# Optimization experiments

Hardware: AMD Instinct MI355X
Metric: run time of the kernel (lower is better)

## Reference

```python
import jax, jax.numpy as jnp
import numpy as np

T, B, I, H, L = 512, 4096, 23, 20, 2  # seq len, batch, input dim, hidden dim, num layers


def setup_inputs() -> dict:
    key = jax.random.key(0)
    ks = jax.random.split(key, 13)
    s = 1.0 / np.sqrt(H)  # pytorch default uniform bound scale (use normal*s for simplicity)
    f32 = jnp.float32
    return {
        "x": jax.random.normal(ks[0], (T, B, I), f32),
        "h0": jax.random.normal(ks[1], (L, B, H), f32),
        "c0": jax.random.normal(ks[2], (L, B, H), f32),
        "W_ih0": jax.random.normal(ks[3], (4 * H, I), f32) * s,
        "W_hh0": jax.random.normal(ks[4], (4 * H, H), f32) * s,
        "b_ih0": jax.random.normal(ks[5], (4 * H,), f32) * s,
        "b_hh0": jax.random.normal(ks[6], (4 * H,), f32) * s,
        "W_ih1": jax.random.normal(ks[7], (4 * H, H), f32) * s,
        "W_hh1": jax.random.normal(ks[8], (4 * H, H), f32) * s,
        "b_ih1": jax.random.normal(ks[9], (4 * H,), f32) * s,
        "b_hh1": jax.random.normal(ks[10], (4 * H,), f32) * s,
        "W_lin": jax.random.normal(ks[11], (1, H), f32) * s,
        "b_lin": jax.random.normal(ks[12], (1,), f32) * s,
    }


def _lstm_layer(xs, h0, c0, W_ih, W_hh, b_ih, b_hh):
    # Precompute input contributions for all timesteps at once: [T, B, 4H]
    xg = jnp.einsum('tbi,gi->tbg', xs, W_ih) + b_ih + b_hh

    def step(carry, xg_t):
        h, c = carry
        gates = xg_t + h @ W_hh.T          # [B, 4H]
        i, f, g, o = jnp.split(gates, 4, axis=-1)  # pytorch gate order: i, f, g, o
        c = jax.nn.sigmoid(f) * c + jax.nn.sigmoid(i) * jnp.tanh(g)
        h = jax.nn.sigmoid(o) * jnp.tanh(c)
        return (h, c), h

    _, hs = jax.lax.scan(step, (h0, c0), xg)
    return hs  # [T, B, H]


def reference(x, h0, c0, W_ih0, W_hh0, b_ih0, b_hh0, W_ih1, W_hh1, b_ih1, b_hh1, W_lin, b_lin):
    out = _lstm_layer(x, h0[0], c0[0], W_ih0, W_hh0, b_ih0, b_hh0)
    out = _lstm_layer(out, h0[1], c0[1], W_ih1, W_hh1, b_ih1, b_hh1)
    y = jax.nn.relu(out)                   # relu(lstm output), [T, B, H]
    # lin applied then time-index 6 selected; equivalent (and cheaper) to index first
    z6 = y[6] @ W_lin.T + b_lin            # [B, 1]
    return jax.nn.relu(z6)
```

## Files before the change

### kernel.cpp

```cpp
#include <hip/hip_runtime.h>
#include <math.h>


constexpr int kT  = 7;
constexpr int kI  = 23;
constexpr int kH  = 20;
constexpr int kG  = 80;
constexpr int kBT = 8;
constexpr int kThreads = 320;

__device__ __forceinline__ float sigm(float v) {
    return __builtin_amdgcn_rcpf(1.0f + __builtin_amdgcn_exp2f(v * -1.44269504f));
}
__device__ __forceinline__ float tanh_(float v) {
    return 1.0f - 2.0f * __builtin_amdgcn_rcpf(__builtin_amdgcn_exp2f(v * 2.88539008f) + 1.0f);
}
template<int J>
__device__ __forceinline__ float qb(float v) {
    return __int_as_float(__builtin_amdgcn_mov_dpp(__float_as_int(v), J * 0x55, 0xF, 0xF, true));
}
__device__ __forceinline__ void lstm_update(float a, float& c, float& h) {
    const float gi = qb<0>(a);
    const float gf = qb<1>(a);
    const float gg = qb<2>(a);
    const float go = qb<3>(a);
    c = sigm(gf) * c + sigm(gi) * tanh_(gg);
    h = sigm(go) * tanh_(c);
}

__global__ __launch_bounds__(kThreads, 3) void lstm7_kernel(
    const float* __restrict__ x,
    const float* __restrict__ h0,
    const float* __restrict__ c0,
    const float* __restrict__ Wih0,
    const float* __restrict__ Whh0,
    const float* __restrict__ bih0,
    const float* __restrict__ bhh0,
    const float* __restrict__ Wih1,
    const float* __restrict__ Whh1,
    const float* __restrict__ bih1,
    const float* __restrict__ bhh1,
    const float* __restrict__ Wlin,
    const float* __restrict__ blin,
    float* __restrict__ out,
    int B)
{
    __shared__ __align__(16) float xS[kT][kI][kBT];
    __shared__ __align__(16) float h1S[2][kH][kBT];
    __shared__ __align__(16) float h2S[2][kH][kBT];

    const int tid = threadIdx.x;
    const int b0  = blockIdx.x * kBT;
    const int bp  = tid / kG;
    const int q   = tid & 3;
    const int u   = (tid % kG) >> 2;
    const int grow = q * kH + u;
    const int bb  = bp * 2;

    for (int idx = tid; idx < kT * kI * kBT; idx += kThreads) {
        const int t = idx / (kI * kBT);
        const int r = idx % (kI * kBT);
        const int i = r / kBT;
        const int b = r % kBT;
        xS[t][i][b] = x[((size_t)t * B + b0 + b) * kI + i];
    }
    if (tid < kH * kBT) {
        const int uu = tid / kBT, b = tid % kBT;
        h1S[0][uu][b] = h0[(size_t)(b0 + b) * kH + uu];
        h2S[0][uu][b] = h0[(size_t)(B + b0 + b) * kH + uu];
    }

    float wA[kI], wB[kH], wC[kH], wD[kH];
    {
        const float* pa = Wih0 + grow * kI;
#pragma unroll
        for (int k = 0; k < kI; ++k) wA[k] = pa[k];
        const float4* pb = reinterpret_cast<const float4*>(Whh0 + grow * kH);
        const float4* pc = reinterpret_cast<const float4*>(Wih1 + grow * kH);
        const float4* pd = reinterpret_cast<const float4*>(Whh1 + grow * kH);
#pragma unroll
        for (int j = 0; j < 5; ++j) {
            const float4 vb = pb[j], vc = pc[j], vd = pd[j];
            wB[4*j] = vb.x; wB[4*j+1] = vb.y; wB[4*j+2] = vb.z; wB[4*j+3] = vb.w;
            wC[4*j] = vc.x; wC[4*j+1] = vc.y; wC[4*j+2] = vc.z; wC[4*j+3] = vc.w;
            wD[4*j] = vd.x; wD[4*j+1] = vd.y; wD[4*j+2] = vd.z; wD[4*j+3] = vd.w;
        }
    }
    const float bias1 = bih0[grow] + bhh0[grow];
    const float bias2 = bih1[grow] + bhh1[grow];

    float2 c1, c2;
    c1.x = c0[(size_t)(b0 + bb) * kH + u];
    c1.y = c0[(size_t)(b0 + bb + 1) * kH + u];
    c2.x = c0[(size_t)(B + b0 + bb) * kH + u];
    c2.y = c0[(size_t)(B + b0 + bb + 1) * kH + u];

    __syncthreads();

#pragma unroll
    for (int t = 0; t < kT; ++t) {
        const int rb = t & 1, wb = rb ^ 1;

        float a0 = bias1, a1 = bias1, e0 = 0.f, e1 = 0.f;
#pragma unroll
        for (int k = 0; k < kI; ++k) {
            const float2 v = *reinterpret_cast<const float2*>(&xS[t][k][bb]);
            if (k & 1) { e0 = fmaf(wA[k], v.x, e0); e1 = fmaf(wA[k], v.y, e1); }
            else       { a0 = fmaf(wA[k], v.x, a0); a1 = fmaf(wA[k], v.y, a1); }
        }
#pragma unroll
        for (int k = 0; k < kH; ++k) {
            const float2 v = *reinterpret_cast<const float2*>(&h1S[rb][k][bb]);
            if (k & 1) { e0 = fmaf(wB[k], v.x, e0); e1 = fmaf(wB[k], v.y, e1); }
            else       { a0 = fmaf(wB[k], v.x, a0); a1 = fmaf(wB[k], v.y, a1); }
        }
        a0 += e0; a1 += e1;

        {
            float hx, hy;
            lstm_update(a0, c1.x, hx);
            lstm_update(a1, c1.y, hy);
            if (q == 0) *reinterpret_cast<float2*>(&h1S[wb][u][bb]) = make_float2(hx, hy);
        }
        __syncthreads();

        float g0 = bias2, g1 = bias2, f0 = 0.f, f1 = 0.f;
#pragma unroll
        for (int k = 0; k < kH; ++k) {
            const float2 v = *reinterpret_cast<const float2*>(&h1S[wb][k][bb]);
            if (k & 1) { f0 = fmaf(wC[k], v.x, f0); f1 = fmaf(wC[k], v.y, f1); }
            else       { g0 = fmaf(wC[k], v.x, g0); g1 = fmaf(wC[k], v.y, g1); }
        }
#pragma unroll
        for (int k = 0; k < kH; ++k) {
            const float2 v = *reinterpret_cast<const float2*>(&h2S[rb][k][bb]);
            if (k & 1) { f0 = fmaf(wD[k], v.x, f0); f1 = fmaf(wD[k], v.y, f1); }
            else       { g0 = fmaf(wD[k], v.x, g0); g1 = fmaf(wD[k], v.y, g1); }
        }
        g0 += f0; g1 += f1;

        {
            float hx, hy;
            lstm_update(g0, c2.x, hx);
            lstm_update(g1, c2.y, hy);
            if (q == 0) *reinterpret_cast<float2*>(&h2S[wb][u][bb]) = make_float2(hx, hy);
        }
        __syncthreads();
    }

    if (tid < kBT) {
        const int b = tid;
        float acc = blin[0];
#pragma unroll
        for (int uu = 0; uu < kH; ++uu) {
            acc = fmaf(fmaxf(h2S[1][uu][b], 0.0f), Wlin[uu], acc);
        }
        out[b0 + b] = fmaxf(acc, 0.0f);
    }
}

extern "C" void kernel_launch(void* const* d_in, const int* in_sizes, int n_in,
                              void* d_out, int out_size, void* d_ws, size_t ws_size,
                              hipStream_t stream) {
    const float* x    = (const float*)d_in[0];
    const float* h0   = (const float*)d_in[1];
    const float* c0   = (const float*)d_in[2];
    const float* Wih0 = (const float*)d_in[3];
    const float* Whh0 = (const float*)d_in[4];
    const float* bih0 = (const float*)d_in[5];
    const float* bhh0 = (const float*)d_in[6];
    const float* Wih1 = (const float*)d_in[7];
    const float* Whh1 = (const float*)d_in[8];
    const float* bih1 = (const float*)d_in[9];
    const float* bhh1 = (const float*)d_in[10];
    const float* Wlin = (const float*)d_in[11];
    const float* blin = (const float*)d_in[12];
    float* out = (float*)d_out;

    const int B = in_sizes[1] / (2 * kH);
    const int blocks = B / kBT;

    hipLaunchKernelGGL(lstm7_kernel, dim3(blocks), dim3(kThreads), 0, stream,
                       x, h0, c0, Wih0, Whh0, bih0, bhh0,
                       Wih1, Whh1, bih1, bhh1, Wlin, blin, out, B);
}
```

Before: 24.93 us.

## Remap LSTM to single-wavefront blocks with DPP-rotated hidden-state dot products

Each block is now one 64-thread wavefront handling two batch elements, instead of 320 threads handling eight. Each lane computes one primary gate row plus a redundant secondary row. Lanes in a quad load a float4 slice of the hidden state and pass it around with DPP rotations, so each lane makes fewer LDS reads; weights are stored in the matching rotated order. The layer-0 input projection for all 7 steps is computed before the recurrence, and single-buffered shared state relies on in-order execution within one wave. The costs are redundant math for gate rows 16-19, higher register pressure, and four times as many blocks.

Result: slower. 70.74 us (+183.7%).

```diff
diff --git a/kernel.cpp b/kernel.cpp
--- a/kernel.cpp
+++ b/kernel.cpp
@@ -2,12 +2,11 @@
 #include <math.h>
 
 
-constexpr int kT  = 7;
-constexpr int kI  = 23;
-constexpr int kH  = 20;
-constexpr int kG  = 80;
-constexpr int kBT = 8;
-constexpr int kThreads = 320;
+constexpr int kT = 7;
+constexpr int kI = 23;
+constexpr int kH = 20;
+constexpr int kE = 2;
+constexpr int kThreads = 64;
 
 __device__ __forceinline__ float sigm(float v) {
     return __builtin_amdgcn_rcpf(1.0f + __builtin_amdgcn_exp2f(v * -1.44269504f));
@@ -19,16 +18,66 @@
 __device__ __forceinline__ float qb(float v) {
     return __int_as_float(__builtin_amdgcn_mov_dpp(__float_as_int(v), J * 0x55, 0xF, 0xF, true));
 }
+__device__ __forceinline__ float rotl(float v) {
+    return __int_as_float(__builtin_amdgcn_mov_dpp(__float_as_int(v), 0x39, 0xF, 0xF, true));
+}
+__device__ __forceinline__ float4 rot4(float4 v) {
+    return make_float4(rotl(v.x), rotl(v.y), rotl(v.z), rotl(v.w));
+}
 __device__ __forceinline__ void lstm_update(float a, float& c, float& h) {
-    const float gi = qb<0>(a);
-    const float gf = qb<1>(a);
-    const float gg = qb<2>(a);
-    const float go = qb<3>(a);
+    const float gi = qb<0>(a), gf = qb<1>(a), gg = qb<2>(a), go = qb<3>(a);
     c = sigm(gf) * c + sigm(gi) * tanh_(gg);
     h = sigm(go) * tanh_(c);
 }
 
-__global__ __launch_bounds__(kThreads, 3) void lstm7_kernel(
+#define DOT_STEP4(o)                                                 \
+    p0 = fmaf(wp[o+0], v.x, p0); p1 = fmaf(wp[o+1], v.y, p1);        \
+    s0 = fmaf(ws[o+0], v.x, s0); s1 = fmaf(ws[o+1], v.y, s1);        \
+    p0 = fmaf(wp[o+2], v.z, p0); p1 = fmaf(wp[o+3], v.w, p1);        \
+    s0 = fmaf(ws[o+2], v.z, s0); s1 = fmaf(ws[o+3], v.w, s1);
+
+__device__ __forceinline__ void dot20x2(const float* __restrict__ row,
+                                        const float* wp, const float* ws,
+                                        int q4, float& rp, float& rs)
+{
+    float4 v = *reinterpret_cast<const float4*>(row + q4);
+    float p0 = 0.f, p1 = 0.f, s0 = 0.f, s1 = 0.f;
+    DOT_STEP4(0)  v = rot4(v);
+    DOT_STEP4(4)  v = rot4(v);
+    DOT_STEP4(8)  v = rot4(v);
+    DOT_STEP4(12)
+    const float4 t = *reinterpret_cast<const float4*>(row + 16);
+    p0 = fmaf(wp[16], t.x, p0); p1 = fmaf(wp[17], t.y, p1);
+    s0 = fmaf(ws[16], t.x, s0); s1 = fmaf(ws[17], t.y, s1);
+    p0 = fmaf(wp[18], t.z, p0); p1 = fmaf(wp[19], t.w, p1);
+    s0 = fmaf(ws[18], t.z, s0); s1 = fmaf(ws[19], t.w, s1);
+    rp = p0 + p1; rs = s0 + s1;
+}
+
+__device__ __forceinline__ void dot24x2(const float* __restrict__ row,
+                                        const float* wp, const float* ws,
+                                        int q4, float& rp, float& rs)
+{
+    float4 v = *reinterpret_cast<const float4*>(row + q4);
+    float p0 = 0.f, p1 = 0.f, s0 = 0.f, s1 = 0.f;
+    DOT_STEP4(0)  v = rot4(v);
+    DOT_STEP4(4)  v = rot4(v);
+    DOT_STEP4(8)  v = rot4(v);
+    DOT_STEP4(12)
+    const float4 t4 = *reinterpret_cast<const float4*>(row + 16);
+    p0 = fmaf(wp[16], t4.x, p0); p1 = fmaf(wp[17], t4.y, p1);
+    s0 = fmaf(ws[16], t4.x, s0); s1 = fmaf(ws[17], t4.y, s1);
+    p0 = fmaf(wp[18], t4.z, p0); p1 = fmaf(wp[19], t4.w, p1);
+    s0 = fmaf(ws[18], t4.z, s0); s1 = fmaf(ws[19], t4.w, s1);
+    const float4 t5 = *reinterpret_cast<const float4*>(row + 20);
+    p0 = fmaf(wp[20], t5.x, p0); p1 = fmaf(wp[21], t5.y, p1);
+    s0 = fmaf(ws[20], t5.x, s0); s1 = fmaf(ws[21], t5.y, s1);
+    p0 = fmaf(wp[22], t5.z, p0); p1 = fmaf(wp[23], t5.w, p1);
+    s0 = fmaf(ws[22], t5.z, s0); s1 = fmaf(ws[23], t5.w, s1);
+    rp = p0 + p1; rs = s0 + s1;
+}
+
+__global__ __launch_bounds__(kThreads, 2) void lstm7_kernel(
     const float* __restrict__ x,
     const float* __restrict__ h0,
     const float* __restrict__ c0,
@@ -45,117 +94,143 @@
     float* __restrict__ out,
     int B)
 {
-    __shared__ __align__(16) float xS[kT][kI][kBT];
-    __shared__ __align__(16) float h1S[2][kH][kBT];
-    __shared__ __align__(16) float h2S[2][kH][kBT];
+    __shared__ __align__(16) float xL[kE][kT][24];
+    __shared__ __align__(16) float h1S[kE][24];
+    __shared__ __align__(16) float h2S[kE][24];
 
     const int tid = threadIdx.x;
-    const int b0  = blockIdx.x * kBT;
-    const int bp  = tid / kG;
+    const int b0  = blockIdx.x * kE;
     const int q   = tid & 3;
-    const int u   = (tid % kG) >> 2;
-    const int grow = q * kH + u;
-    const int bb  = bp * 2;
-
-    for (int idx = tid; idx < kT * kI * kBT; idx += kThreads) {
-        const int t = idx / (kI * kBT);
-        const int r = idx % (kI * kBT);
-        const int i = r / kBT;
-        const int b = r % kBT;
-        xS[t][i][b] = x[((size_t)t * B + b0 + b) * kI + i];
-    }
-    if (tid < kH * kBT) {
-        const int uu = tid / kBT, b = tid % kBT;
-        h1S[0][uu][b] = h0[(size_t)(b0 + b) * kH + uu];
-        h2S[0][uu][b] = h0[(size_t)(B + b0 + b) * kH + uu];
-    }
-
-    float wA[kI], wB[kH], wC[kH], wD[kH];
+    const int u   = tid >> 2;
+    const int su  = 16 + (u & 3);
+    const int gp  = q * kH + u;
+    const int gs  = q * kH + su;
+    const int q4  = q * 4;
+
+    for (int idx = tid; idx < kE * kT * 24; idx += kThreads) {
+        const int e = idx / (kT * 24);
+        const int r = idx % (kT * 24);
+        const int t = r / 24;
+        const int i = r % 24;
+        xL[e][t][i] = (i < kI) ? x[((size_t)t * B + b0 + e) * kI + i] : 0.0f;
+    }
+    if (tid < kE * kH) {
+        const int e = tid / kH, uu = tid % kH;
+        h1S[e][uu] = h0[(size_t)(b0 + e) * kH + uu];
+        h2S[e][uu] = h0[((size_t)B + b0 + e) * kH + uu];
+    }
+    __syncthreads();
+
+    float xgp0[kT], xgp1[kT], xgs0[kT], xgs1[kT];
     {
-        const float* pa = Wih0 + grow * kI;
-#pragma unroll
-        for (int k = 0; k < kI; ++k) wA[k] = pa[k];
-        const float4* pb = reinterpret_cast<const float4*>(Whh0 + grow * kH);
-        const float4* pc = reinterpret_cast<const float4*>(Wih1 + grow * kH);
-        const float4* pd = reinterpret_cast<const float4*>(Whh1 + grow * kH);
-#pragma unroll
-        for (int j = 0; j < 5; ++j) {
-            const float4 vb = pb[j], vc = pc[j], vd = pd[j];
-            wB[4*j] = vb.x; wB[4*j+1] = vb.y; wB[4*j+2] = vb.z; wB[4*j+3] = vb.w;
-            wC[4*j] = vc.x; wC[4*j+1] = vc.y; wC[4*j+2] = vc.z; wC[4*j+3] = vc.w;
-            wD[4*j] = vd.x; wD[4*j+1] = vd.y; wD[4*j+2] = vd.z; wD[4*j+3] = vd.w;
-        }
-    }
-    const float bias1 = bih0[grow] + bhh0[grow];
-    const float bias2 = bih1[grow] + bhh1[grow];
-
-    float2 c1, c2;
-    c1.x = c0[(size_t)(b0 + bb) * kH + u];
-    c1.y = c0[(size_t)(b0 + bb + 1) * kH + u];
-    c2.x = c0[(size_t)(B + b0 + bb) * kH + u];
-    c2.y = c0[(size_t)(B + b0 + bb + 1) * kH + u];
-
-    __syncthreads();
+        float wAp[24], wAs[24];
+        const float* Ap = Wih0 + gp * kI;
+        const float* As = Wih0 + gs * kI;
+#pragma unroll
+        for (int r = 0; r < 4; ++r) {
+            const int c = (q + r) & 3;
+#pragma unroll
+            for (int j = 0; j < 4; ++j) {
+                wAp[4*r + j] = Ap[4*c + j];
+                wAs[4*r + j] = As[4*c + j];
+            }
+        }
+#pragma unroll
+        for (int j = 0; j < 7; ++j) { wAp[16 + j] = Ap[16 + j]; wAs[16 + j] = As[16 + j]; }
+        wAp[23] = 0.0f; wAs[23] = 0.0f;
+        const float b1p = bih0[gp] + bhh0[gp];
+        const float b1s = bih0[gs] + bhh0[gs];
+#pragma unroll
+        for (int t = 0; t < kT; ++t) {
+            float dp, ds;
+            dot24x2(&xL[0][t][0], wAp, wAs, q4, dp, ds);
+            xgp0[t] = b1p + dp; xgs0[t] = b1s + ds;
+            dot24x2(&xL[1][t][0], wAp, wAs, q4, dp, ds);
+            xgp1[t] = b1p + dp; xgs1[t] = b1s + ds;
+        }
+    }
+
+    float wBp[kH], wCp[kH], wDp[kH], wBs[kH], wCs[kH], wDs[kH];
+    {
+        const float4* PB = reinterpret_cast<const float4*>(Whh0 + gp * kH);
+        const float4* PC = reinterpret_cast<const float4*>(Wih1 + gp * kH);
+        const float4* PD = reinterpret_cast<const float4*>(Whh1 + gp * kH);
+        const float4* SB = reinterpret_cast<const float4*>(Whh0 + gs * kH);
+        const float4* SC = reinterpret_cast<const float4*>(Wih1 + gs * kH);
+        const float4* SD = reinterpret_cast<const float4*>(Whh1 + gs * kH);
+#pragma unroll
+        for (int r = 0; r < 4; ++r) {
+            const int c = (q + r) & 3;
+            const float4 vb = PB[c], vc = PC[c], vd = PD[c];
+            const float4 ub = SB[c], uc = SC[c], ud = SD[c];
+            wBp[4*r+0]=vb.x; wBp[4*r+1]=vb.y; wBp[4*r+2]=vb.z; wBp[4*r+3]=vb.w;
+            wCp[4*r+0]=vc.x; wCp[4*r+1]=vc.y; wCp[4*r+2]=vc.z; wCp[4*r+3]=vc.w;
+            wDp[4*r+0]=vd.x; wDp[4*r+1]=vd.y; wDp[4*r+2]=vd.z; wDp[4*r+3]=vd.w;
+            wBs[4*r+0]=ub.x; wBs[4*r+1]=ub.y; wBs[4*r+2]=ub.z; wBs[4*r+3]=ub.w;
+            wCs[4*r+0]=uc.x; wCs[4*r+1]=uc.y; wCs[4*r+2]=uc.z; wCs[4*r+3]=uc.w;
+            wDs[4*r+0]=ud.x; wDs[4*r+1]=ud.y; wDs[4*r+2]=ud.z; wDs[4*r+3]=ud.w;
+        }
+        const float4 tb = PB[4], tc = PC[4], td = PD[4];
+        const float4 rb = SB[4], rc = SC[4], rd = SD[4];
+        wBp[16]=tb.x; wBp[17]=tb.y; wBp[18]=tb.z; wBp[19]=tb.w;
+        wCp[16]=tc.x; wCp[17]=tc.y; wCp[18]=tc.z; wCp[19]=tc.w;
+        wDp[16]=td.x; wDp[17]=td.y; wDp[18]=td.z; wDp[19]=td.w;
+        wBs[16]=rb.x; wBs[17]=rb.y; wBs[18]=rb.z; wBs[19]=rb.w;
+        wCs[16]=rc.x; wCs[17]=rc.y; wCs[18]=rc.z; wCs[19]=rc.w;
+        wDs[16]=rd.x; wDs[17]=rd.y; wDs[18]=rd.z; wDs[19]=rd.w;
+    }
+    const float b2p = bih1[gp] + bhh1[gp];
+    const float b2s = bih1[gs] + bhh1[gs];
+
+    float c1p0 = c0[(size_t)(b0 + 0) * kH + u];
+    float c1p1 = c0[(size_t)(b0 + 1) * kH + u];
+    float c2p0 = c0[((size_t)B + b0 + 0) * kH + u];
+    float c2p1 = c0[((size_t)B + b0 + 1) * kH + u];
+    float c1s0 = c0[(size_t)(b0 + 0) * kH + su];
+    float c1s1 = c0[(size_t)(b0 + 1) * kH + su];
+    float c2s0 = c0[((size_t)B + b0 + 0) * kH + su];
+    float c2s1 = c0[((size_t)B + b0 + 1) * kH + su];
 
 #pragma unroll
     for (int t = 0; t < kT; ++t) {
-        const int rb = t & 1, wb = rb ^ 1;
-
-        float a0 = bias1, a1 = bias1, e0 = 0.f, e1 = 0.f;
-#pragma unroll
-        for (int k = 0; k < kI; ++k) {
-            const float2 v = *reinterpret_cast<const float2*>(&xS[t][k][bb]);
-            if (k & 1) { e0 = fmaf(wA[k], v.x, e0); e1 = fmaf(wA[k], v.y, e1); }
-            else       { a0 = fmaf(wA[k], v.x, a0); a1 = fmaf(wA[k], v.y, a1); }
-        }
-#pragma unroll
-        for (int k = 0; k < kH; ++k) {
-            const float2 v = *reinterpret_cast<const float2*>(&h1S[rb][k][bb]);
-            if (k & 1) { e0 = fmaf(wB[k], v.x, e0); e1 = fmaf(wB[k], v.y, e1); }
-            else       { a0 = fmaf(wB[k], v.x, a0); a1 = fmaf(wB[k], v.y, a1); }
-        }
-        a0 += e0; a1 += e1;
-
-        {
-            float hx, hy;
-            lstm_update(a0, c1.x, hx);
-            lstm_update(a1, c1.y, hy);
-            if (q == 0) *reinterpret_cast<float2*>(&h1S[wb][u][bb]) = make_float2(hx, hy);
+        float dp0, ds0, dp1, ds1;
+        dot20x2(&h1S[0][0], wBp, wBs, q4, dp0, ds0);
+        dot20x2(&h1S[1][0], wBp, wBs, q4, dp1, ds1);
+        float h1p0, h1p1, h1s0, h1s1;
+        lstm_update(xgp0[t] + dp0, c1p0, h1p0);
+        lstm_update(xgp1[t] + dp1, c1p1, h1p1);
+        lstm_update(xgs0[t] + ds0, c1s0, h1s0);
+        lstm_update(xgs1[t] + ds1, c1s1, h1s1);
+        if (q == 0) {
+            h1S[0][u] = h1p0; h1S[1][u] = h1p1;
+            if (u < 4) { h1S[0][su] = h1s0; h1S[1][su] = h1s1; }
         }
         __syncthreads();
 
-        float g0 = bias2, g1 = bias2, f0 = 0.f, f1 = 0.f;
-#pragma unroll
-        for (int k = 0; k < kH; ++k) {
-            const float2 v = *reinterpret_cast<const float2*>(&h1S[wb][k][bb]);
-            if (k & 1) { f0 = fmaf(wC[k], v.x, f0); f1 = fmaf(wC[k], v.y, f1); }
-            else       { g0 = fmaf(wC[k], v.x, g0); g1 = fmaf(wC[k], v.y, g1); }
-        }
-#pragma unroll
-        for (int k = 0; k < kH; ++k) {
-            const float2 v = *reinterpret_cast<const float2*>(&h2S[rb][k][bb]);
-            if (k & 1) { f0 = fmaf(wD[k], v.x, f0); f1 = fmaf(wD[k], v.y, f1); }
-            else       { g0 = fmaf(wD[k], v.x, g0); g1 = fmaf(wD[k], v.y, g1); }
-        }
-        g0 += f0; g1 += f1;
-
-        {
-            float hx, hy;
-            lstm_update(g0, c2.x, hx);
-            lstm_update(g1, c2.y, hy);
-            if (q == 0) *reinterpret_cast<float2*>(&h2S[wb][u][bb]) = make_float2(hx, hy);
+        float ap0, as0, ap1, as1, bp0, bs0, bp1, bs1;
+        dot20x2(&h1S[0][0], wCp, wCs, q4, ap0, as0);
+        dot20x2(&h2S[0][0], wDp, wDs, q4, bp0, bs0);
+        dot20x2(&h1S[1][0], wCp, wCs, q4, ap1, as1);
+        dot20x2(&h2S[1][0], wDp, wDs, q4, bp1, bs1);
+        float h2p0, h2p1, h2s0, h2s1;
+        lstm_update(b2p + ap0 + bp0, c2p0, h2p0);
+        lstm_update(b2p + ap1 + bp1, c2p1, h2p1);
+        lstm_update(b2s + as0 + bs0, c2s0, h2s0);
+        lstm_update(b2s + as1 + bs1, c2s1, h2s1);
+        if (q == 0) {
+            h2S[0][u] = h2p0; h2S[1][u] = h2p1;
+            if (u < 4) { h2S[0][su] = h2s0; h2S[1][su] = h2s1; }
         }
         __syncthreads();
     }
 
-    if (tid < kBT) {
-        const int b = tid;
+    if (tid < kE) {
         float acc = blin[0];
 #pragma unroll
         for (int uu = 0; uu < kH; ++uu) {
-            acc = fmaf(fmaxf(h2S[1][uu][b], 0.0f), Wlin[uu], acc);
-        }
-        out[b0 + b] = fmaxf(acc, 0.0f);
+            acc = fmaf(fmaxf(h2S[tid][uu], 0.0f), Wlin[uu], acc);
+        }
+        out[b0 + tid] = fmaxf(acc, 0.0f);
     }
 }
 
@@ -178,7 +253,7 @@
     float* out = (float*)d_out;
 
     const int B = in_sizes[1] / (2 * kH);
-    const int blocks = B / kBT;
+    const int blocks = B / kE;
 
     hipLaunchKernelGGL(lstm7_kernel, dim3(blocks), dim3(kThreads), 0, stream,
                        x, h0, c0, Wih0, Whh0, bih0, bhh0,
```
